# Performance work log

Measured on AMD Instinct MI355X. Metric: run time of the kernel, lower is better.

Reference implementation:

```python
import jax, jax.numpy as jnp
import numpy as np

N = 100000
H1, D1 = 8, 8          # conv1: 8 heads x 8 dims (concat -> 64)
C = 40                 # num_classes, conv2: 1 head
NEG_SLOPE = 0.2


def gat_layer(x, edge_index, W, a_src, a_dst, b, heads, out_dim, concat):
    # x: [N, F_in], W: [F_in, heads*out_dim], a_*: [heads, out_dim], b: [heads*out_dim] or [out_dim]
    h = (x @ W).reshape(-1, heads, out_dim)                 # [N, H, D]
    s_src = jnp.einsum('nhd,hd->nh', h, a_src)              # [N, H]
    s_dst = jnp.einsum('nhd,hd->nh', h, a_dst)              # [N, H]
    src, dst = edge_index[0], edge_index[1]
    e = jax.nn.leaky_relu(s_src[src] + s_dst[dst], NEG_SLOPE)   # [E, H]
    # segment softmax over incoming edges of each dst node
    m = jax.ops.segment_max(e, dst, num_segments=N)         # [N, H]
    e = jnp.exp(e - m[dst])
    z = jax.ops.segment_sum(e, dst, num_segments=N)         # [N, H]
    alpha = e / (z[dst] + 1e-16)                            # [E, H]
    msg = h[src] * alpha[:, :, None]                        # [E, H, D]
    out = jax.ops.segment_sum(msg, dst, num_segments=N)     # [N, H, D]
    if concat:
        out = out.reshape(-1, heads * out_dim)
    else:
        out = out.mean(axis=1)
    return out + b


def setup_inputs() -> dict:
    key = jax.random.key(0)
    ks = jax.random.split(key, 10)
    F_in = 256
    x = jax.random.normal(ks[0], (N, F_in), dtype=jnp.float32)
    edge_index = jax.random.randint(ks[1], (2, 1600000), 0, N, dtype=jnp.int32)
    sc1 = 1.0 / np.sqrt(F_in)
    W1 = jax.random.normal(ks[2], (F_in, H1 * D1), dtype=jnp.float32) * sc1
    a1_src = jax.random.normal(ks[3], (H1, D1), dtype=jnp.float32) * 0.1
    a1_dst = jax.random.normal(ks[4], (H1, D1), dtype=jnp.float32) * 0.1
    b1 = jnp.zeros((H1 * D1,), dtype=jnp.float32)
    sc2 = 1.0 / np.sqrt(H1 * D1)
    W2 = jax.random.normal(ks[5], (H1 * D1, C), dtype=jnp.float32) * sc2
    a2_src = jax.random.normal(ks[6], (1, C), dtype=jnp.float32) * 0.1
    a2_dst = jax.random.normal(ks[7], (1, C), dtype=jnp.float32) * 0.1
    b2 = jnp.zeros((C,), dtype=jnp.float32)
    return {"x": x, "edge_index": edge_index, "W1": W1, "a1_src": a1_src,
            "a1_dst": a1_dst, "b1": b1, "W2": W2, "a2_src": a2_src,
            "a2_dst": a2_dst, "b2": b2}


def reference(x, edge_index, W1, a1_src, a1_dst, b1, W2, a2_src, a2_dst, b2):
    # eval mode: dropout is identity
    h = gat_layer(x, edge_index, W1, a1_src, a1_dst, b1, H1, D1, concat=True)
    h = jax.nn.elu(h)
    out = gat_layer(h, edge_index, W2, a2_src, a2_dst, b2, 1, C, concat=False)
    return jax.nn.log_softmax(out, axis=1)
```

## Files before the change

### kernel.cpp

```cpp
#include <hip/hip_runtime.h>
#include <math.h>

#define BK 10
#define KNODES 1024
#define MAXNB 128

typedef __attribute__((ext_vector_type(8))) short bf16x8;
typedef __attribute__((ext_vector_type(4))) float f32x4;

__device__ __forceinline__ float bf2f(unsigned short u) {
  return __uint_as_float(((unsigned int)u) << 16);
}
__device__ __forceinline__ unsigned short f2bf(float f) {
  unsigned int i = __float_as_uint(f);
  unsigned int r = i + 0x7FFFu + ((i >> 16) & 1u);
  return (unsigned short)(r >> 16);
}

__global__ __launch_bounds__(256) void prep_kernel(
    const float* __restrict__ W1, const float* __restrict__ W2,
    const float* __restrict__ a2s, const float* __restrict__ a2d,
    unsigned short* __restrict__ whi, unsigned short* __restrict__ wlo,
    float* __restrict__ vas, float* __restrict__ vad,
    unsigned short* __restrict__ h1b, unsigned short* __restrict__ h2b,
    float* __restrict__ s1s, float* __restrict__ s2s,
    int* __restrict__ bpos, int capP, int NN) {
  const int blk = blockIdx.x, t = threadIdx.x;
  if (blk == 0 && t < MAXNB) bpos[t] = t * capP;
  if (blk < 32) {
    if (t < 64) {
      int b = blk, lane = t;
      int kt = b >> 2, ct = b & 3;
      int n = lane & 15, g = lane >> 4;
      unsigned short hb[8], lb[8];
#pragma unroll
      for (int j = 0; j < 8; ++j) {
        int k = kt * 32 + g * 8 + j;
        float wv = W1[k * 64 + ct * 16 + n];
        unsigned short hi = f2bf(wv);
        float rem = wv - bf2f(hi);
        hb[j] = hi;
        lb[j] = f2bf(rem);
      }
      size_t base = ((size_t)b * 64 + lane) * 8;
      *(ushort4*)(whi + base)     = make_ushort4(hb[0], hb[1], hb[2], hb[3]);
      *(ushort4*)(whi + base + 4) = make_ushort4(hb[4], hb[5], hb[6], hb[7]);
      *(ushort4*)(wlo + base)     = make_ushort4(lb[0], lb[1], lb[2], lb[3]);
      *(ushort4*)(wlo + base + 4) = make_ushort4(lb[4], lb[5], lb[6], lb[7]);
    }
  } else if (blk == 32) {
    if (t < 64) {
      float s = 0.f, d = 0.f;
      for (int c = 0; c < 40; ++c) {
        float w = W2[t * 40 + c];
        s += w * a2s[c];
        d += w * a2d[c];
      }
      vas[t] = s;
      vad[t] = d;
    }
  } else if (blk == 33) {
    if (t < 64) {
      h1b[(size_t)NN * 64 + t] = 0;
      if (t < 40) h2b[(size_t)NN * 40 + t] = 0;
      if (t < 8)  s1s[(size_t)NN * 8 + t] = -1e30f;
      if (t == 0) s2s[NN] = -1e30f;
    }
  }
}

__global__ __launch_bounds__(256) void gemm1_mfma_kernel(
    const float* __restrict__ x, const unsigned short* __restrict__ whi,
    const unsigned short* __restrict__ wlo, unsigned short* __restrict__ h1b, int N) {
  const int w = threadIdx.x >> 6, lane = threadIdx.x & 63;
  const int m = lane & 15, g = lane >> 4;
  const int rbase = blockIdx.x * 64 + w * 16;
  int arow = rbase + m;
  if (arow >= N) arow = N - 1;
  const float* xrow = x + (size_t)arow * 256 + g * 8;
  f32x4 acc[4] = {{0.f, 0.f, 0.f, 0.f}, {0.f, 0.f, 0.f, 0.f},
                  {0.f, 0.f, 0.f, 0.f}, {0.f, 0.f, 0.f, 0.f}};
#pragma unroll
  for (int kt = 0; kt < 8; ++kt) {
    float4 a0 = *(const float4*)(xrow + kt * 32);
    float4 a1 = *(const float4*)(xrow + kt * 32 + 4);
    float av[8] = {a0.x, a0.y, a0.z, a0.w, a1.x, a1.y, a1.z, a1.w};
    bf16x8 ahi, alo;
#pragma unroll
    for (int j = 0; j < 8; ++j) {
      unsigned int u = __float_as_uint(av[j]);
      unsigned short hi = (unsigned short)(u >> 16);
      float rem = av[j] - bf2f(hi);
      ahi[j] = (short)hi;
      alo[j] = (short)(__float_as_uint(rem) >> 16);
    }
    const unsigned short* wp = whi + ((size_t)(kt * 4) * 64 + lane) * 8;
    const unsigned short* lp = wlo + ((size_t)(kt * 4) * 64 + lane) * 8;
#pragma unroll
    for (int ct = 0; ct < 4; ++ct) {
      bf16x8 bh = *(const bf16x8*)(wp + (size_t)ct * 64 * 8);
      bf16x8 bl = *(const bf16x8*)(lp + (size_t)ct * 64 * 8);
      acc[ct] = __builtin_amdgcn_mfma_f32_16x16x32_bf16(ahi, bh, acc[ct], 0, 0, 0);
      acc[ct] = __builtin_amdgcn_mfma_f32_16x16x32_bf16(alo, bh, acc[ct], 0, 0, 0);
      acc[ct] = __builtin_amdgcn_mfma_f32_16x16x32_bf16(ahi, bl, acc[ct], 0, 0, 0);
    }
  }
#pragma unroll
  for (int r = 0; r < 4; ++r) {
    int ro = rbase + g * 4 + r;
    if (ro < N) {
#pragma unroll
      for (int ct = 0; ct < 4; ++ct)
        h1b[(size_t)ro * 64 + ct * 16 + m] = f2bf(acc[ct][r]);
    }
  }
}

__global__ void s1_kernel(const unsigned short* __restrict__ h1b,
                          const float* __restrict__ a_src,
                          const float* __restrict__ a_dst, float* __restrict__ s_src,
                          float* __restrict__ s_dst, int N8) {
  int id = blockIdx.x * blockDim.x + threadIdx.x;
  if (id >= N8) return;
  int h = id & 7;
  uint4 raw = *(const uint4*)(h1b + (size_t)id * 8);
  float hv[8];
  hv[0] = bf2f(raw.x & 0xffff); hv[1] = bf2f(raw.x >> 16);
  hv[2] = bf2f(raw.y & 0xffff); hv[3] = bf2f(raw.y >> 16);
  hv[4] = bf2f(raw.z & 0xffff); hv[5] = bf2f(raw.z >> 16);
  hv[6] = bf2f(raw.w & 0xffff); hv[7] = bf2f(raw.w >> 16);
  float ss = 0.f, sd = 0.f;
#pragma unroll
  for (int d = 0; d < 8; ++d) {
    ss = fmaf(hv[d], a_src[h * 8 + d], ss);
    sd = fmaf(hv[d], a_dst[h * 8 + d], sd);
  }
  s_src[id] = ss;
  s_dst[id] = sd;
}

__global__ __launch_bounds__(256) void bin_kernel(const int* __restrict__ src,
                                                  const int* __restrict__ dst,
                                                  int* __restrict__ bpos,
                                                  unsigned int* __restrict__ payload,
                                                  int E, int NB, int capP) {
  __shared__ int hist[MAXNB], soff[MAXNB], base[MAXNB], rnk[MAXNB];
  __shared__ unsigned int stage[4096];
  const int t = threadIdx.x;
  const int e0 = blockIdx.x * 4096;
  if (t < MAXNB) { hist[t] = 0; rnk[t] = 0; }
  __syncthreads();
  for (int j = t; j < 4096; j += 256) {
    int e = e0 + j;
    if (e < E) atomicAdd(&hist[dst[e] >> BK], 1);
  }
  __syncthreads();
  if (t == 0) {
    int acc = 0;
    for (int b = 0; b < NB; ++b) { soff[b] = acc; acc += hist[b]; }
  }
  __syncthreads();
  if (t < NB) {
    int c = hist[t];
    base[t] = c ? atomicAdd(&bpos[t], c) : 0;
  }
  __syncthreads();
  for (int j = t; j < 4096; j += 256) {
    int e = e0 + j;
    if (e < E) {
      int d = dst[e];
      int b = d >> BK;
      int s = src[e];
      int r = atomicAdd(&rnk[b], 1);
      stage[soff[b] + r] = (((unsigned)(d & (KNODES - 1))) << 17) | (unsigned)s;
    }
  }
  __syncthreads();
  int wave = t >> 6, lane = t & 63;
  for (int b = wave; b < NB; b += 4) {
    int len = hist[b], bs = soff[b], gb = base[b];
    int lim = (b + 1) * capP;
    for (int j = lane; j < len; j += 64)
      if (gb + j < lim) payload[gb + j] = stage[bs + j];
  }
}

__global__ __launch_bounds__(1024) void fill2_kernel(const unsigned int* __restrict__ payload,
                                                     const int* __restrict__ bpos,
                                                     int* __restrict__ col,
                                                     int* __restrict__ rbeg,
                                                     int* __restrict__ rend,
                                                     int capP, int NN) {
  __shared__ int cnt[KNODES], scn[KNODES], pos[KNODES];
  const int b = blockIdx.x, t = threadIdx.x;
  cnt[t] = 0;
  __syncthreads();
  const int beg = b * capP;
  int len = bpos[b] - beg;
  if (len > capP) len = capP;
  for (int j = t; j < len; j += 1024) atomicAdd(&cnt[payload[beg + j] >> 17], 1);
  __syncthreads();
  const int myc = cnt[t];
  const int padc = (myc + 7) & ~7;
  scn[t] = padc;
  __syncthreads();
  for (int off = 1; off < 1024; off <<= 1) {
    int v = (t >= off) ? scn[t - off] : 0;
    __syncthreads();
    scn[t] += v;
    __syncthreads();
  }
  const int mystart = b * (capP + 8 * KNODES) + scn[t] - padc;
  const int n = (b << BK) + t;
  if (n < NN) { rbeg[n] = mystart; rend[n] = mystart + padc; }
  pos[t] = mystart;
  __syncthreads();
  for (int j = t; j < len; j += 1024) {
    unsigned int pay = payload[beg + j];
    int p = atomicAdd(&pos[pay >> 17], 1);
    col[p] = (int)(pay & 0x1FFFF);
  }
  __syncthreads();
  for (int j = mystart + myc; j < mystart + padc; ++j) col[j] = NN;
}

__global__ __launch_bounds__(256) void agg1_kernel(
    const int* __restrict__ rbeg, const int* __restrict__ rend,
    const int* __restrict__ col,
    const float* __restrict__ s_src, const float* __restrict__ s_dst,
    const unsigned short* __restrict__ h1b, const float* __restrict__ b1,
    const float* __restrict__ vas, const float* __restrict__ vad,
    unsigned short* __restrict__ helub, float* __restrict__ s2s,
    float* __restrict__ s2d, int N) {
  int wv = threadIdx.x >> 6;
  int l  = threadIdx.x & 63;
  int n  = blockIdx.x * 4 + wv;
  if (n >= N) return;
  const int q  = l >> 3;
  const int hh = l & 7;
  const float sdq = s_dst[n * 8 + hh];
  const int beg = __builtin_amdgcn_readfirstlane(rbeg[n]);
  const int end = __builtin_amdgcn_readfirstlane(rend[n]);
  float z = 0.f, acc = 0.f;
  int e = beg;
  if (((end - beg) >> 3) & 1) {
    int4 ia = *(const int4*)(col + e);
    int4 ib = *(const int4*)(col + e + 4);
    int myidx = col[e + q];
    float pv = s_src[(unsigned)myidx * 8u + (unsigned)hh];
    float tt = pv + sdq;
    tt = fmaxf(tt, 0.2f * tt);
    float w = __expf(tt);
    z += w;
    int idxs[8] = {ia.x, ia.y, ia.z, ia.w, ib.x, ib.y, ib.z, ib.w};
#pragma unroll
    for (int j = 0; j < 8; ++j) {
      float wj = __shfl(w, j * 8 + q, 64);
      unsigned short g = h1b[(unsigned)idxs[j] * 64u + (unsigned)l];
      acc = fmaf(wj, bf2f(g), acc);
    }
    e += 8;
  }
  for (; e < end; e += 16) {
    int4 ia = *(const int4*)(col + e);
    int4 ib = *(const int4*)(col + e + 4);
    int4 ic = *(const int4*)(col + e + 8);
    int4 id = *(const int4*)(col + e + 12);
    int my0 = col[e + q];
    int my1 = col[e + 8 + q];
    float pv0 = s_src[(unsigned)my0 * 8u + (unsigned)hh];
    float pv1 = s_src[(unsigned)my1 * 8u + (unsigned)hh];
    int idxs[16] = {ia.x, ia.y, ia.z, ia.w, ib.x, ib.y, ib.z, ib.w,
                    ic.x, ic.y, ic.z, ic.w, id.x, id.y, id.z, id.w};
    unsigned short gg[16];
#pragma unroll
    for (int j = 0; j < 16; ++j) gg[j] = h1b[(unsigned)idxs[j] * 64u + (unsigned)l];
    float t0 = pv0 + sdq; t0 = fmaxf(t0, 0.2f * t0); float w0 = __expf(t0);
    float t1 = pv1 + sdq; t1 = fmaxf(t1, 0.2f * t1); float w1 = __expf(t1);
    z += w0 + w1;
#pragma unroll
    for (int j = 0; j < 8; ++j) {
      float wj = __shfl(w0, j * 8 + q, 64);
      acc = fmaf(wj, bf2f(gg[j]), acc);
    }
#pragma unroll
    for (int j = 0; j < 8; ++j) {
      float wj = __shfl(w1, j * 8 + q, 64);
      acc = fmaf(wj, bf2f(gg[8 + j]), acc);
    }
  }
  z += __shfl_xor(z, 8); z += __shfl_xor(z, 16); z += __shfl_xor(z, 32);
  float zf = __shfl(z, 9 * q, 64);
  float v = acc / (zf + 1e-16f) + b1[l];
  v = v > 0.f ? v : (__expf(v) - 1.f);
  helub[(size_t)n * 64 + l] = f2bf(v);
  float ps = v * vas[l];
  float pd = v * vad[l];
  for (int off = 32; off > 0; off >>= 1) {
    ps += __shfl_xor(ps, off);
    pd += __shfl_xor(pd, off);
  }
  if (l == 0) { s2s[n] = ps; s2d[n] = pd; }
}

__global__ __launch_bounds__(320) void gemm2_kernel(const unsigned short* __restrict__ heb,
                                                    const float* __restrict__ W2,
                                                    unsigned short* __restrict__ h2b, int N) {
  __shared__ float xs[64][132];
  __shared__ float ws[64][40];
  const int r0 = blockIdx.x * 128;
  const int t  = threadIdx.x;
  const int ty = t / 10;
  const int tx = t % 10;
  for (int idx = t; idx < 1024; idx += 320) {
    int row = idx >> 3;
    int k8  = (idx & 7) << 3;
    uint4 raw = make_uint4(0, 0, 0, 0);
    if (r0 + row < N) raw = *(const uint4*)(heb + (size_t)(r0 + row) * 64 + k8);
    xs[k8 + 0][row] = bf2f(raw.x & 0xffff); xs[k8 + 1][row] = bf2f(raw.x >> 16);
    xs[k8 + 2][row] = bf2f(raw.y & 0xffff); xs[k8 + 3][row] = bf2f(raw.y >> 16);
    xs[k8 + 4][row] = bf2f(raw.z & 0xffff); xs[k8 + 5][row] = bf2f(raw.z >> 16);
    xs[k8 + 6][row] = bf2f(raw.w & 0xffff); xs[k8 + 7][row] = bf2f(raw.w >> 16);
  }
  for (int idx = t; idx < 640; idx += 320) {
    int k  = idx / 10;
    int c4 = (idx % 10) << 2;
    *(float4*)(&ws[k][c4]) = *(const float4*)(W2 + k * 40 + c4);
  }
  __syncthreads();
  float acc[4][4] = {};
#pragma unroll 8
  for (int k = 0; k < 64; ++k) {
    float4 xa = *(const float4*)(&xs[k][ty << 2]);
    float4 wb = *(const float4*)(&ws[k][tx << 2]);
    float xv[4] = {xa.x, xa.y, xa.z, xa.w};
    float wv[4] = {wb.x, wb.y, wb.z, wb.w};
#pragma unroll
    for (int i = 0; i < 4; ++i)
#pragma unroll
      for (int j = 0; j < 4; ++j) acc[i][j] = fmaf(xv[i], wv[j], acc[i][j]);
  }
#pragma unroll
  for (int i = 0; i < 4; ++i) {
    int r = r0 + (ty << 2) + i;
    if (r < N) {
      ushort4 o;
      o.x = f2bf(acc[i][0]); o.y = f2bf(acc[i][1]);
      o.z = f2bf(acc[i][2]); o.w = f2bf(acc[i][3]);
      *(ushort4*)(h2b + (size_t)r * 40 + (tx << 2)) = o;
    }
  }
}

__global__ __launch_bounds__(256) void agg2_kernel(
    const int* __restrict__ rbeg, const int* __restrict__ rend,
    const int* __restrict__ col,
    const float* __restrict__ s2s, const float* __restrict__ s2d,
    const unsigned short* __restrict__ h2b, const float* __restrict__ b2,
    float* __restrict__ out, int N) {
  int wv = threadIdx.x >> 6;
  int l  = threadIdx.x & 63;
  int n  = blockIdx.x * 4 + wv;
  if (n >= N) return;
  const int q = l >> 3;
  const bool act = (l < 40);
  const unsigned lc = act ? (unsigned)l : 0u;
  const float sdv = s2d[n];
  const int beg = __builtin_amdgcn_readfirstlane(rbeg[n]);
  const int end = __builtin_amdgcn_readfirstlane(rend[n]);
  float z = 0.f, acc = 0.f;
  int e = beg;
  if (((end - beg) >> 3) & 1) {
    int4 ia = *(const int4*)(col + e);
    int4 ib = *(const int4*)(col + e + 4);
    int myidx = col[e + q];
    float pv = s2s[myidx];
    float tt = pv + sdv;
    tt = fmaxf(tt, 0.2f * tt);
    float w = __expf(tt);
    z += w;
    int idxs[8] = {ia.x, ia.y, ia.z, ia.w, ib.x, ib.y, ib.z, ib.w};
#pragma unroll
    for (int j = 0; j < 8; ++j) {
      float wj = __shfl(w, j * 8, 64);
      unsigned short g = h2b[(unsigned)idxs[j] * 40u + lc];
      acc = fmaf(wj, bf2f(g), acc);
    }
    e += 8;
  }
  for (; e < end; e += 16) {
    int4 ia = *(const int4*)(col + e);
    int4 ib = *(const int4*)(col + e + 4);
    int4 ic = *(const int4*)(col + e + 8);
    int4 id = *(const int4*)(col + e + 12);
    int my0 = col[e + q];
    int my1 = col[e + 8 + q];
    float pv0 = s2s[my0];
    float pv1 = s2s[my1];
    int idxs[16] = {ia.x, ia.y, ia.z, ia.w, ib.x, ib.y, ib.z, ib.w,
                    ic.x, ic.y, ic.z, ic.w, id.x, id.y, id.z, id.w};
    unsigned short gg[16];
#pragma unroll
    for (int j = 0; j < 16; ++j) gg[j] = h2b[(unsigned)idxs[j] * 40u + lc];
    float t0 = pv0 + sdv; t0 = fmaxf(t0, 0.2f * t0); float w0 = __expf(t0);
    float t1 = pv1 + sdv; t1 = fmaxf(t1, 0.2f * t1); float w1 = __expf(t1);
    z += w0 + w1;
#pragma unroll
    for (int j = 0; j < 8; ++j) {
      float wj = __shfl(w0, j * 8, 64);
      acc = fmaf(wj, bf2f(gg[j]), acc);
    }
#pragma unroll
    for (int j = 0; j < 8; ++j) {
      float wj = __shfl(w1, j * 8, 64);
      acc = fmaf(wj, bf2f(gg[8 + j]), acc);
    }
  }
  z += __shfl_xor(z, 8); z += __shfl_xor(z, 16); z += __shfl_xor(z, 32);
  float v = act ? (acc / (z + 1e-16f) + b2[l]) : -1e30f;
  float m = v;
  for (int off = 32; off > 0; off >>= 1) m = fmaxf(m, __shfl_xor(m, off));
  float ex = act ? __expf(v - m) : 0.f;
  float s = ex;
  for (int off = 32; off > 0; off >>= 1) s += __shfl_xor(s, off);
  if (act) out[(size_t)n * 40 + l] = v - m - logf(s);
}

extern "C" void kernel_launch(void* const* d_in, const int* in_sizes, int n_in,
                              void* d_out, int out_size, void* d_ws, size_t ws_size,
                              hipStream_t stream) {
  const float* x   = (const float*)d_in[0];
  const int*   ei  = (const int*)d_in[1];
  const float* W1  = (const float*)d_in[2];
  const float* a1s = (const float*)d_in[3];
  const float* a1d = (const float*)d_in[4];
  const float* b1  = (const float*)d_in[5];
  const float* W2  = (const float*)d_in[6];
  const float* a2s = (const float*)d_in[7];
  const float* a2d = (const float*)d_in[8];
  const float* b2  = (const float*)d_in[9];
  float* out = (float*)d_out;
  (void)n_in; (void)out_size; (void)ws_size;

  const int NN = in_sizes[0] / 256;
  const int E  = in_sizes[1] / 2;
  const int NB = (NN + KNODES - 1) >> BK;
  const int* esrc = ei;
  const int* edst = ei + E;

  int capP = (E + NB - 1) / NB;
  capP += capP / 4 + capP / 16 + 512;
  capP = (capP + 15) & ~15;

  char* p = (char*)d_ws;
  auto alloc = [&](size_t bytes) -> char* {
    char* q = p;
    p += (bytes + 255) & ~(size_t)255;
    return q;
  };
  unsigned short* h1b   = (unsigned short*)alloc((size_t)(NN + 1) * 64 * 2);
  unsigned short* helub = (unsigned short*)alloc((size_t)NN * 64 * 2);
  unsigned short* h2b   = (unsigned short*)alloc((size_t)(NN + 1) * 40 * 2);
  float* s1s  = (float*)alloc((size_t)(NN + 1) * 8 * 4);
  float* s1d  = (float*)alloc((size_t)NN * 8 * 4);
  float* s2s  = (float*)alloc((size_t)(NN + 1) * 4);
  float* s2d  = (float*)alloc((size_t)NN * 4);
  int*   rbeg = (int*)alloc((size_t)NN * 4);
  int*   rend = (int*)alloc((size_t)NN * 4);
  int*   bpos = (int*)alloc(MAXNB * 4);
  unsigned int* payload = (unsigned int*)alloc((size_t)NB * capP * 4);
  int*   col  = (int*)alloc((size_t)NB * (capP + 8 * KNODES) * 4);
  float* vas  = (float*)alloc(64 * 4);
  float* vad  = (float*)alloc(64 * 4);
  unsigned short* w1hi = (unsigned short*)alloc(32 * 64 * 8 * 2);
  unsigned short* w1lo = (unsigned short*)alloc(32 * 64 * 8 * 2);

  prep_kernel<<<34, 256, 0, stream>>>(W1, W2, a2s, a2d, w1hi, w1lo, vas, vad,
                                      h1b, h2b, s1s, s2s, bpos, capP, NN);
  bin_kernel<<<(E + 4095) / 4096, 256, 0, stream>>>(esrc, edst, bpos, payload, E, NB, capP);
  fill2_kernel<<<NB, 1024, 0, stream>>>(payload, bpos, col, rbeg, rend, capP, NN);
  gemm1_mfma_kernel<<<(NN + 63) / 64, 256, 0, stream>>>(x, w1hi, w1lo, h1b, NN);
  s1_kernel<<<(NN * 8 + 255) / 256, 256, 0, stream>>>(h1b, a1s, a1d, s1s, s1d, NN * 8);
  agg1_kernel<<<(NN + 3) / 4, 256, 0, stream>>>(rbeg, rend, col, s1s, s1d, h1b, b1,
                                                vas, vad, helub, s2s, s2d, NN);
  gemm2_kernel<<<(NN + 127) / 128, 320, 0, stream>>>(helub, W2, h2b, NN);
  agg2_kernel<<<(NN + 3) / 4, 256, 0, stream>>>(rbeg, rend, col, s2s, s2d, h2b, b2, out, NN);
}
```

Measured before the change: 365.6 us.

## Fuse attention scores into gemm1 epilogue and move gemm2 to split-bf16 MFMA

The per-head attention dot products for layer 1 are now computed in the gemm1 MFMA epilogue with lane shuffles, which removes the separate s1_kernel and its re-read of h1. The FP32 LDS-tiled gemm2 is replaced by a bf16 MFMA kernel that uses hi/lo split W2 weights, padded from 40 to 48 columns and prepared in extra prep blocks. Both aggregation kernels also get a second accumulator to shorten the FMA dependency chain. One side effect is that layer-1 scores now come from the fp32 accumulators rather than the bf16-rounded h1, which slightly changes numerics.

```diff
diff --git a/kernel.cpp b/kernel.cpp
--- a/kernel.cpp
+++ b/kernel.cpp
@@ -21,6 +21,7 @@
     const float* __restrict__ W1, const float* __restrict__ W2,
     const float* __restrict__ a2s, const float* __restrict__ a2d,
     unsigned short* __restrict__ whi, unsigned short* __restrict__ wlo,
+    unsigned short* __restrict__ w2hi, unsigned short* __restrict__ w2lo,
     float* __restrict__ vas, float* __restrict__ vad,
     unsigned short* __restrict__ h1b, unsigned short* __restrict__ h2b,
     float* __restrict__ s1s, float* __restrict__ s2s,
@@ -66,12 +67,37 @@
       if (t < 8)  s1s[(size_t)NN * 8 + t] = -1e30f;
       if (t == 0) s2s[NN] = -1e30f;
     }
+  } else if (blk >= 34 && blk < 40) {
+    if (t < 64) {
+      int b = blk - 34;
+      int kt = b / 3, ct = b % 3;
+      int n = t & 15, g = t >> 4;
+      unsigned short hb[8], lb[8];
+#pragma unroll
+      for (int j = 0; j < 8; ++j) {
+        int k = kt * 32 + g * 8 + j;
+        int c = ct * 16 + n;
+        float wv = (c < 40) ? W2[k * 40 + c] : 0.f;
+        unsigned short hi = f2bf(wv);
+        float rem = wv - bf2f(hi);
+        hb[j] = hi;
+        lb[j] = f2bf(rem);
+      }
+      size_t base = ((size_t)b * 64 + t) * 8;
+      *(ushort4*)(w2hi + base)     = make_ushort4(hb[0], hb[1], hb[2], hb[3]);
+      *(ushort4*)(w2hi + base + 4) = make_ushort4(hb[4], hb[5], hb[6], hb[7]);
+      *(ushort4*)(w2lo + base)     = make_ushort4(lb[0], lb[1], lb[2], lb[3]);
+      *(ushort4*)(w2lo + base + 4) = make_ushort4(lb[4], lb[5], lb[6], lb[7]);
+    }
   }
 }
 
 __global__ __launch_bounds__(256) void gemm1_mfma_kernel(
     const float* __restrict__ x, const unsigned short* __restrict__ whi,
-    const unsigned short* __restrict__ wlo, unsigned short* __restrict__ h1b, int N) {
+    const unsigned short* __restrict__ wlo,
+    const float* __restrict__ a_src, const float* __restrict__ a_dst,
+    unsigned short* __restrict__ h1b,
+    float* __restrict__ s_src, float* __restrict__ s_dst, int N) {
   const int w = threadIdx.x >> 6, lane = threadIdx.x & 63;
   const int m = lane & 15, g = lane >> 4;
   const int rbase = blockIdx.x * 64 + w * 16;
@@ -114,29 +140,38 @@
         h1b[(size_t)ro * 64 + ct * 16 + m] = f2bf(acc[ct][r]);
     }
   }
-}
-
-__global__ void s1_kernel(const unsigned short* __restrict__ h1b,
-                          const float* __restrict__ a_src,
-                          const float* __restrict__ a_dst, float* __restrict__ s_src,
-                          float* __restrict__ s_dst, int N8) {
-  int id = blockIdx.x * blockDim.x + threadIdx.x;
-  if (id >= N8) return;
-  int h = id & 7;
-  uint4 raw = *(const uint4*)(h1b + (size_t)id * 8);
-  float hv[8];
-  hv[0] = bf2f(raw.x & 0xffff); hv[1] = bf2f(raw.x >> 16);
-  hv[2] = bf2f(raw.y & 0xffff); hv[3] = bf2f(raw.y >> 16);
-  hv[4] = bf2f(raw.z & 0xffff); hv[5] = bf2f(raw.z >> 16);
-  hv[6] = bf2f(raw.w & 0xffff); hv[7] = bf2f(raw.w >> 16);
-  float ss = 0.f, sd = 0.f;
-#pragma unroll
-  for (int d = 0; d < 8; ++d) {
-    ss = fmaf(hv[d], a_src[h * 8 + d], ss);
-    sd = fmaf(hv[d], a_dst[h * 8 + d], sd);
-  }
-  s_src[id] = ss;
-  s_dst[id] = sd;
+  float a1sv[4], a1dv[4];
+#pragma unroll
+  for (int ct = 0; ct < 4; ++ct) {
+    a1sv[ct] = a_src[ct * 16 + m];
+    a1dv[ct] = a_dst[ct * 16 + m];
+  }
+#pragma unroll
+  for (int r = 0; r < 4; ++r) {
+    float ps[4], pd[4];
+#pragma unroll
+    for (int ct = 0; ct < 4; ++ct) {
+      ps[ct] = acc[ct][r] * a1sv[ct];
+      pd[ct] = acc[ct][r] * a1dv[ct];
+    }
+#pragma unroll
+    for (int off = 1; off < 8; off <<= 1) {
+#pragma unroll
+      for (int ct = 0; ct < 4; ++ct) {
+        ps[ct] += __shfl_xor(ps[ct], off);
+        pd[ct] += __shfl_xor(pd[ct], off);
+      }
+    }
+    int ro = rbase + g * 4 + r;
+    if ((m & 7) == 0 && ro < N) {
+      int hb2 = m >> 3;
+#pragma unroll
+      for (int ct = 0; ct < 4; ++ct) {
+        s_src[(size_t)ro * 8 + ct * 2 + hb2] = ps[ct];
+        s_dst[(size_t)ro * 8 + ct * 2 + hb2] = pd[ct];
+      }
+    }
+  }
 }
 
 __global__ __launch_bounds__(256) void bin_kernel(const int* __restrict__ src,
@@ -241,7 +276,7 @@
   const float sdq = s_dst[n * 8 + hh];
   const int beg = __builtin_amdgcn_readfirstlane(rbeg[n]);
   const int end = __builtin_amdgcn_readfirstlane(rend[n]);
-  float z = 0.f, acc = 0.f;
+  float z = 0.f, acc = 0.f, acc2 = 0.f;
   int e = beg;
   if (((end - beg) >> 3) & 1) {
     int4 ia = *(const int4*)(col + e);
@@ -286,9 +321,10 @@
 #pragma unroll
     for (int j = 0; j < 8; ++j) {
       float wj = __shfl(w1, j * 8 + q, 64);
-      acc = fmaf(wj, bf2f(gg[8 + j]), acc);
-    }
-  }
+      acc2 = fmaf(wj, bf2f(gg[8 + j]), acc2);
+    }
+  }
+  acc += acc2;
   z += __shfl_xor(z, 8); z += __shfl_xor(z, 16); z += __shfl_xor(z, 32);
   float zf = __shfl(z, 9 * q, 64);
   float v = acc / (zf + 1e-16f) + b1[l];
@@ -303,51 +339,37 @@
   if (l == 0) { s2s[n] = ps; s2d[n] = pd; }
 }
 
-__global__ __launch_bounds__(320) void gemm2_kernel(const unsigned short* __restrict__ heb,
-                                                    const float* __restrict__ W2,
-                                                    unsigned short* __restrict__ h2b, int N) {
-  __shared__ float xs[64][132];
-  __shared__ float ws[64][40];
-  const int r0 = blockIdx.x * 128;
-  const int t  = threadIdx.x;
-  const int ty = t / 10;
-  const int tx = t % 10;
-  for (int idx = t; idx < 1024; idx += 320) {
-    int row = idx >> 3;
-    int k8  = (idx & 7) << 3;
-    uint4 raw = make_uint4(0, 0, 0, 0);
-    if (r0 + row < N) raw = *(const uint4*)(heb + (size_t)(r0 + row) * 64 + k8);
-    xs[k8 + 0][row] = bf2f(raw.x & 0xffff); xs[k8 + 1][row] = bf2f(raw.x >> 16);
-    xs[k8 + 2][row] = bf2f(raw.y & 0xffff); xs[k8 + 3][row] = bf2f(raw.y >> 16);
-    xs[k8 + 4][row] = bf2f(raw.z & 0xffff); xs[k8 + 5][row] = bf2f(raw.z >> 16);
-    xs[k8 + 6][row] = bf2f(raw.w & 0xffff); xs[k8 + 7][row] = bf2f(raw.w >> 16);
-  }
-  for (int idx = t; idx < 640; idx += 320) {
-    int k  = idx / 10;
-    int c4 = (idx % 10) << 2;
-    *(float4*)(&ws[k][c4]) = *(const float4*)(W2 + k * 40 + c4);
-  }
-  __syncthreads();
-  float acc[4][4] = {};
-#pragma unroll 8
-  for (int k = 0; k < 64; ++k) {
-    float4 xa = *(const float4*)(&xs[k][ty << 2]);
-    float4 wb = *(const float4*)(&ws[k][tx << 2]);
-    float xv[4] = {xa.x, xa.y, xa.z, xa.w};
-    float wv[4] = {wb.x, wb.y, wb.z, wb.w};
-#pragma unroll
-    for (int i = 0; i < 4; ++i)
-#pragma unroll
-      for (int j = 0; j < 4; ++j) acc[i][j] = fmaf(xv[i], wv[j], acc[i][j]);
-  }
-#pragma unroll
-  for (int i = 0; i < 4; ++i) {
-    int r = r0 + (ty << 2) + i;
-    if (r < N) {
-      ushort4 o;
-      o.x = f2bf(acc[i][0]); o.y = f2bf(acc[i][1]);
-      o.z = f2bf(acc[i][2]); o.w = f2bf(acc[i][3]);
-      *(ushort4*)(h2b + (size_t)r * 40 + (tx << 2)) = o;
+__global__ __launch_bounds__(256) void gemm2_mfma_kernel(
+    const unsigned short* __restrict__ heb, const unsigned short* __restrict__ w2hi,
+    const unsigned short* __restrict__ w2lo, unsigned short* __restrict__ h2b, int N) {
+  const int w = threadIdx.x >> 6, lane = threadIdx.x & 63;
+  const int m = lane & 15, g = lane >> 4;
+  const int rbase = blockIdx.x * 64 + w * 16;
+  int arow = rbase + m;
+  if (arow >= N) arow = N - 1;
+  const unsigned short* hrow = heb + (size_t)arow * 64 + g * 8;
+  f32x4 acc[3] = {{0.f, 0.f, 0.f, 0.f}, {0.f, 0.f, 0.f, 0.f}, {0.f, 0.f, 0.f, 0.f}};
+#pragma unroll
+  for (int kt = 0; kt < 2; ++kt) {
+    bf16x8 a = *(const bf16x8*)(hrow + kt * 32);
+#pragma unroll
+    for (int ct = 0; ct < 3; ++ct) {
+      int b = kt * 3 + ct;
+      bf16x8 bh = *(const bf16x8*)(w2hi + ((size_t)b * 64 + lane) * 8);
+      bf16x8 bl = *(const bf16x8*)(w2lo + ((size_t)b * 64 + lane) * 8);
+      acc[ct] = __builtin_amdgcn_mfma_f32_16x16x32_bf16(a, bh, acc[ct], 0, 0, 0);
+      acc[ct] = __builtin_amdgcn_mfma_f32_16x16x32_bf16(a, bl, acc[ct], 0, 0, 0);
+    }
+  }
+#pragma unroll
+  for (int r = 0; r < 4; ++r) {
+    int ro = rbase + g * 4 + r;
+    if (ro < N) {
+#pragma unroll
+      for (int ct = 0; ct < 3; ++ct) {
+        int c = ct * 16 + m;
+        if (c < 40) h2b[(size_t)ro * 40 + c] = f2bf(acc[ct][r]);
+      }
     }
   }
 }
@@ -368,7 +390,7 @@
   const float sdv = s2d[n];
   const int beg = __builtin_amdgcn_readfirstlane(rbeg[n]);
   const int end = __builtin_amdgcn_readfirstlane(rend[n]);
-  float z = 0.f, acc = 0.f;
+  float z = 0.f, acc = 0.f, acc2 = 0.f;
   int e = beg;
   if (((end - beg) >> 3) & 1) {
     int4 ia = *(const int4*)(col + e);
@@ -413,9 +435,10 @@
 #pragma unroll
     for (int j = 0; j < 8; ++j) {
       float wj = __shfl(w1, j * 8, 64);
-      acc = fmaf(wj, bf2f(gg[8 + j]), acc);
-    }
-  }
+      acc2 = fmaf(wj, bf2f(gg[8 + j]), acc2);
+    }
+  }
+  acc += acc2;
   z += __shfl_xor(z, 8); z += __shfl_xor(z, 16); z += __shfl_xor(z, 32);
   float v = act ? (acc / (z + 1e-16f) + b2[l]) : -1e30f;
   float m = v;
@@ -474,15 +497,17 @@
   float* vad  = (float*)alloc(64 * 4);
   unsigned short* w1hi = (unsigned short*)alloc(32 * 64 * 8 * 2);
   unsigned short* w1lo = (unsigned short*)alloc(32 * 64 * 8 * 2);
-
-  prep_kernel<<<34, 256, 0, stream>>>(W1, W2, a2s, a2d, w1hi, w1lo, vas, vad,
-                                      h1b, h2b, s1s, s2s, bpos, capP, NN);
+  unsigned short* w2hi = (unsigned short*)alloc(6 * 64 * 8 * 2);
+  unsigned short* w2lo = (unsigned short*)alloc(6 * 64 * 8 * 2);
+
+  prep_kernel<<<40, 256, 0, stream>>>(W1, W2, a2s, a2d, w1hi, w1lo, w2hi, w2lo,
+                                      vas, vad, h1b, h2b, s1s, s2s, bpos, capP, NN);
   bin_kernel<<<(E + 4095) / 4096, 256, 0, stream>>>(esrc, edst, bpos, payload, E, NB, capP);
   fill2_kernel<<<NB, 1024, 0, stream>>>(payload, bpos, col, rbeg, rend, capP, NN);
-  gemm1_mfma_kernel<<<(NN + 63) / 64, 256, 0, stream>>>(x, w1hi, w1lo, h1b, NN);
-  s1_kernel<<<(NN * 8 + 255) / 256, 256, 0, stream>>>(h1b, a1s, a1d, s1s, s1d, NN * 8);
+  gemm1_mfma_kernel<<<(NN + 63) / 64, 256, 0, stream>>>(x, w1hi, w1lo, a1s, a1d,
+                                                        h1b, s1s, s1d, NN);
   agg1_kernel<<<(NN + 3) / 4, 256, 0, stream>>>(rbeg, rend, col, s1s, s1d, h1b, b1,
                                                 vas, vad, helub, s2s, s2d, NN);
-  gemm2_kernel<<<(NN + 127) / 128, 320, 0, stream>>>(helub, W2, h2b, NN);
+  gemm2_mfma_kernel<<<(NN + 63) / 64, 256, 0, stream>>>(helub, w2hi, w2lo, h2b, NN);
   agg2_kernel<<<(NN + 3) / 4, 256, 0, stream>>>(rbeg, rend, col, s2s, s2d, h2b, b2, out, NN);
 }
```

New measurement: 358.6 us. Within noise of the previous version (-1.9%).
